# Kernel tuning notes

Hardware: AMD Instinct MI355X
Metric: run time of the kernel (lower is better)

## Reference

```python
import jax, jax.numpy as jnp
import numpy as np

N, E, F, D, EH, G, L, NG = 50000, 800000, 32, 32, 96, 128, 3, 500


def setup_inputs() -> dict:
    key = jax.random.key(0)
    ks = iter(jax.random.split(key, 32))
    w = lambda shape: jax.random.normal(next(ks), shape, dtype=jnp.float32) * 0.05
    inp = {
        "node_features": jax.random.normal(next(ks), (N, F), dtype=jnp.float32),
        "enc_W": w((F, D)), "enc_b": w((D,)),
        "msg_W1": w((L, 2 * D, EH)), "msg_b1": w((L, EH)),
        "msg_W2": w((L, EH, EH)), "msg_b2": w((L, EH)),
        "rmsg_W1": w((L, 2 * D, EH)), "rmsg_b1": w((L, EH)),
        "rmsg_W2": w((L, EH, EH)), "rmsg_b2": w((L, EH)),
        "gru_Wih": w((L, 3 * D, EH)), "gru_Whh": w((L, 3 * D, D)),
        "gru_bih": w((L, 3 * D)), "gru_bhh": w((L, 3 * D)),
        "agg_W1": w((D, 2 * G)), "agg_b1": w((2 * G,)),
        "agg_W2": w((G, G)), "agg_b2": w((G,)),
        "from_idx": jax.random.randint(next(ks), (E,), 0, N),
        "to_idx": jax.random.randint(next(ks), (E,), 0, N),
        "graph_idx": jnp.sort(jax.random.randint(next(ks), (N,), 0, NG)),
        "n_graphs": NG,
    }
    return inp


def _mlp(x, W1, b1, W2, b2):
    # Linear -> ReLU -> Linear (message net)
    return jax.nn.relu(x @ W1 + b1) @ W2 + b2


def _gru_step(x, h, Wih, Whh, bih, bhh):
    # torch nn.GRU single-step, gate order r, z, n
    gi = x @ Wih.T + bih  # [n, 3D]
    gh = h @ Whh.T + bhh  # [n, 3D]
    ir, iz, inn = jnp.split(gi, 3, axis=-1)
    hr, hz, hn = jnp.split(gh, 3, axis=-1)
    r = jax.nn.sigmoid(ir + hr)
    z = jax.nn.sigmoid(iz + hz)
    n = jnp.tanh(inn + r * hn)
    return (1.0 - z) * n + z * h


def _forward(node_features, enc_W, enc_b, msg_W1, msg_b1, msg_W2, msg_b2,
             rmsg_W1, rmsg_b1, rmsg_W2, rmsg_b2, gru_Wih, gru_Whh, gru_bih, gru_bhh,
             agg_W1, agg_b1, agg_W2, agg_b2, from_idx, to_idx, graph_idx, n_graphs):
    # GraphEncoder: single Linear
    h = node_features @ enc_W + enc_b  # [N, D]
    n_nodes = h.shape[0]
    n_layers = msg_W1.shape[0]
    for l in range(n_layers):  # small fixed layer count
        fs = h[from_idx]  # [E, D] gather
        ts = h[to_idx]    # [E, D] gather
        # forward-direction messages: gather -> concat -> MLP -> scatter_add to to_idx
        m = _mlp(jnp.concatenate([fs, ts], axis=-1), msg_W1[l], msg_b1[l], msg_W2[l], msg_b2[l])
        agg = jax.ops.segment_sum(m, to_idx, num_segments=n_nodes)
        # reverse direction: roles of from/to swapped, scatter to from_idx
        mr = _mlp(jnp.concatenate([ts, fs], axis=-1), rmsg_W1[l], rmsg_b1[l], rmsg_W2[l], rmsg_b2[l])
        agg = agg + jax.ops.segment_sum(mr, from_idx, num_segments=n_nodes)
        # node update via GRU (aggregated messages as input, node states as hidden)
        h = _gru_step(agg, h, gru_Wih[l], gru_Whh[l], gru_bih[l], gru_bhh[l])
    # GraphAggregator: gated node transform + scatter_add by graph, then Linear
    g = h @ agg_W1 + agg_b1  # [N, 2G]
    gdim = agg_W2.shape[0]
    gated = jax.nn.sigmoid(g[:, :gdim]) * g[:, gdim:]
    graph_states = jax.ops.segment_sum(gated, graph_idx, num_segments=n_graphs)  # [n_graphs, G]
    return graph_states @ agg_W2 + agg_b2


def reference(node_features, enc_W, enc_b, msg_W1, msg_b1, msg_W2, msg_b2,
              rmsg_W1, rmsg_b1, rmsg_W2, rmsg_b2, gru_Wih, gru_Whh, gru_bih, gru_bhh,
              agg_W1, agg_b1, agg_W2, agg_b2, from_idx, to_idx, graph_idx, n_graphs):
    return _forward(node_features, enc_W, enc_b, msg_W1, msg_b1, msg_W2, msg_b2,
                    rmsg_W1, rmsg_b1, rmsg_W2, rmsg_b2, gru_Wih, gru_Whh, gru_bih, gru_bhh,
                    agg_W1, agg_b1, agg_W2, agg_b2, from_idx, to_idx, graph_idx, n_graphs)
```

## Files before the change

### kernel.cpp

```cpp
#include <hip/hip_runtime.h>

#define SB 512

typedef __attribute__((ext_vector_type(8))) short short8;
typedef __attribute__((ext_vector_type(4))) float f32x4;

__device__ inline unsigned short f2bf(float f) {
    unsigned u = __float_as_uint(f);
    unsigned r = (u + 0x7fffu + ((u >> 16) & 1u)) >> 16;
    return (unsigned short)r;
}
__device__ inline unsigned pack2bf(float x, float y) {
    return (unsigned)f2bf(x) | ((unsigned)f2bf(y) << 16);
}

__global__ void count_rank_kernel(const int* __restrict__ from_idx, const int* __restrict__ to_idx,
                                  int* __restrict__ cnt_to, int* __restrict__ cnt_from,
                                  int* __restrict__ rank_to, int* __restrict__ rank_from, int E) {
    int e = blockIdx.x * blockDim.x + threadIdx.x;
    if (e >= E) return;
    int f = from_idx[e], t = to_idx[e];
    rank_to[e] = atomicAdd(&cnt_to[t], 1);
    rank_from[e] = atomicAdd(&cnt_from[f], 1);
}

__global__ void __launch_bounds__(SB) scanA_kernel(const int* __restrict__ cnt_to,
                                                   const int* __restrict__ cnt_from,
                                                   int* __restrict__ bsum, int nblk, int N) {
    const int* cnt = blockIdx.y ? cnt_from : cnt_to;
    __shared__ int s[SB];
    int tid = threadIdx.x;
    int i = blockIdx.x * SB + tid;
    s[tid] = (i < N) ? cnt[i] : 0;
    __syncthreads();
    for (int d = SB / 2; d > 0; d >>= 1) {
        if (tid < d) s[tid] += s[tid + d];
        __syncthreads();
    }
    if (tid == 0) bsum[blockIdx.y * nblk + blockIdx.x] = s[0];
}

__global__ void scanB_kernel(int* __restrict__ bsum, int* __restrict__ bbase,
                             int* __restrict__ off_to, int* __restrict__ off_from,
                             int nblk, int N) {
    int tid = threadIdx.x;
    if (tid < 2) {
        const int* bs = bsum + tid * nblk;
        int* bb = bbase + tid * nblk;
        int run = 0;
        for (int i = 0; i < nblk; ++i) { bb[i] = run; run += bs[i]; }
        if (tid == 0) off_to[N] = run; else off_from[N] = run;
    }
}

__global__ void __launch_bounds__(SB) scanC_kernel(const int* __restrict__ cnt_to,
                                                   const int* __restrict__ cnt_from,
                                                   const int* __restrict__ bbase,
                                                   int* __restrict__ off_to, int* __restrict__ off_from,
                                                   int nblk, int N) {
    const int* cnt = blockIdx.y ? cnt_from : cnt_to;
    int* off = blockIdx.y ? off_from : off_to;
    __shared__ int s[SB];
    int tid = threadIdx.x;
    int i = blockIdx.x * SB + tid;
    int v = (i < N) ? cnt[i] : 0;
    s[tid] = v;
    __syncthreads();
    for (int d = 1; d < SB; d <<= 1) {
        int t = s[tid];
        int add = (tid >= d) ? s[tid - d] : 0;
        __syncthreads();
        s[tid] = t + add;
        __syncthreads();
    }
    if (i < N) off[i] = s[tid] - v + bbase[blockIdx.y * nblk + blockIdx.x];
}

__global__ void fill_kernel(const int* __restrict__ from_idx, const int* __restrict__ to_idx,
                            const int* __restrict__ off_to, const int* __restrict__ off_from,
                            const int* __restrict__ rank_to, const int* __restrict__ rank_from,
                            int* __restrict__ list_to, int* __restrict__ list_from, int E) {
    int e = blockIdx.x * blockDim.x + threadIdx.x;
    if (e >= E) return;
    int f = from_idx[e], t = to_idx[e];
    list_to[off_to[t] + rank_to[e]] = f;
    list_from[off_from[f] + rank_from[e]] = t;
}

__global__ void transpose_whh(const float* __restrict__ Whh, float* __restrict__ WhhT) {
    int idx = blockIdx.x * 256 + threadIdx.x;
    if (idx >= 3 * 32 * 96) return;
    int l = idx / 3072, r = idx % 3072;
    int j = r / 96, k = r % 96;
    WhhT[idx] = Whh[l * 3072 + k * 32 + j];
}

__global__ void compose_kernel(const float* __restrict__ W2, const float* __restrict__ rW2,
                               const float* __restrict__ Wih,
                               const float* __restrict__ b2, const float* __restrict__ rb2,
                               float* __restrict__ M1, float* __restrict__ M2,
                               float* __restrict__ v12) {
    int l = blockIdx.x / 97, j = blockIdx.x % 97;
    int k = threadIdx.x;
    const float* wih = Wih + l * 9216 + k * 96;
    if (j < 96) {
        const float* w2  = W2 + l * 9216 + j * 96;
        const float* rw2 = rW2 + l * 9216 + j * 96;
        float a1 = 0.f, a2 = 0.f;
        for (int m = 0; m < 96; ++m) {
            float wv = wih[m];
            a1 = fmaf(w2[m], wv, a1);
            a2 = fmaf(rw2[m], wv, a2);
        }
        M1[l * 9216 + j * 96 + k] = a1;
        M2[l * 9216 + j * 96 + k] = a2;
    } else {
        const float* bb = b2 + l * 96;
        const float* rbb = rb2 + l * 96;
        float a1 = 0.f, a2 = 0.f;
        for (int m = 0; m < 96; ++m) {
            float wv = wih[m];
            a1 = fmaf(bb[m], wv, a1);
            a2 = fmaf(rbb[m], wv, a2);
        }
        v12[l * 192 + k] = a1;
        v12[l * 192 + 96 + k] = a2;
    }
}

__global__ void repack_kernel(const float* __restrict__ M1, const float* __restrict__ M2,
                              const float* __restrict__ WhhT,
                              const float* __restrict__ W1f, const float* __restrict__ W1r,
                              unsigned* __restrict__ M1bc, unsigned* __restrict__ M2bc,
                              unsigned* __restrict__ Whhbc, unsigned* __restrict__ W1bc) {
    int idx = blockIdx.x * 256 + threadIdx.x;
    if (idx < 13824) {
        int l = idx / 4608, r = idx % 4608, c = r / 48, wd = r % 48;
        const float* src = M1 + l * 9216;
        M1bc[idx] = pack2bf(src[(2 * wd) * 96 + c], src[(2 * wd + 1) * 96 + c]);
    } else if (idx < 27648) {
        int j = idx - 13824;
        int l = j / 4608, r = j % 4608, c = r / 48, wd = r % 48;
        const float* src = M2 + l * 9216;
        M2bc[j] = pack2bf(src[(2 * wd) * 96 + c], src[(2 * wd + 1) * 96 + c]);
    } else if (idx < 32256) {
        int j = idx - 27648;
        int l = j / 1536, r = j % 1536, c = r / 16, wd = r % 16;
        const float* src = WhhT + l * 3072;
        Whhbc[j] = pack2bf(src[(2 * wd) * 96 + c], src[(2 * wd + 1) * 96 + c]);
    } else if (idx < 32256 + 18432) {
        int j = idx - 32256;
        int l = j / 6144, r = j % 6144, C = r / 16, wd = r % 16;
        const float* src; int col, rb;
        if (C < 96)       { src = W1f + l * 6144; col = C;       rb = 0;  }
        else if (C < 192) { src = W1f + l * 6144; col = C - 96;  rb = 32; }
        else if (C < 288) { src = W1r + l * 6144; col = C - 192; rb = 0;  }
        else              { src = W1r + l * 6144; col = C - 288; rb = 32; }
        W1bc[j] = pack2bf(src[(rb + 2 * wd) * 96 + col], src[(rb + 2 * wd + 1) * 96 + col]);
    }
}

__global__ void __launch_bounds__(256) enc_gemm(const float* __restrict__ IN,
                                                const float* __restrict__ W, const float* __restrict__ bias,
                                                float* __restrict__ OUT, unsigned short* __restrict__ hb16, int N) {
    __shared__ float tile[64][33];
    int n0 = blockIdx.x * 64, tid = threadIdx.x;
    for (int idx = tid; idx < 64 * 32; idx += 256) {
        int r = idx >> 5, c = idx & 31;
        int n = n0 + r;
        tile[r][c] = (n < N) ? IN[(long)n * 32 + c] : 0.f;
    }
    __syncthreads();
    int lane = tid & 63;
    int w = __builtin_amdgcn_readfirstlane(tid >> 6);
    float acc[8] = {0};
    const float* Wp = W + w * 8;
#pragma unroll 4
    for (int j = 0; j < 32; ++j) {
        float a = tile[lane][j];
#pragma unroll
        for (int c = 0; c < 8; ++c) acc[c] = fmaf(a, Wp[j * 32 + c], acc[c]);
    }
    int n = n0 + lane;
    if (n >= N) return;
    float* outp = OUT + (long)n * 32 + w * 8;
    unsigned short* bp = hb16 + (long)n * 32 + w * 8;
#pragma unroll
    for (int c = 0; c < 8; ++c) {
        float v = acc[c] + bias[w * 8 + c];
        outp[c] = v;
        bp[c] = f2bf(v);
    }
}

__global__ void __launch_bounds__(512) proj_mfma(
    const unsigned* __restrict__ hb, const unsigned* __restrict__ W1bc,
    const float* __restrict__ b1f, const float* __restrict__ b1r,
    unsigned short* __restrict__ PaF16, float* __restrict__ PbF,
    unsigned short* __restrict__ PaR16, float* __restrict__ PbR, int N)
{
    int tid = threadIdx.x;
    int lane = tid & 63;
    int w = __builtin_amdgcn_readfirstlane(tid >> 6);
    int nt = w >> 1, cg = w & 1;
    int kgrp = lane >> 4, l15 = lane & 15;
    int ntile = blockIdx.x * 64 + nt * 16;
    int arow = ntile + l15;
    long arc = (arow < N) ? arow : (N - 1);
    short8 a = *(const short8*)(hb + arc * 16 + kgrp * 4);

    unsigned short* Pa16 = cg ? PaR16 : PaF16;
    float* Pb = cg ? PbR : PbF;
    const float* b1 = cg ? b1r : b1f;

    f32x4 acc[12];
#pragma unroll
    for (int ct = 0; ct < 12; ++ct) {
        int col = cg * 192 + ct * 16 + l15;
        short8 b = *(const short8*)(W1bc + (long)col * 16 + kgrp * 4);
        acc[ct] = __builtin_amdgcn_mfma_f32_16x16x32_bf16(a, b, (f32x4){0.f,0.f,0.f,0.f}, 0, 0, 0);
    }
    int nbase = ntile + kgrp * 4;
#pragma unroll
    for (int ct = 0; ct < 6; ++ct) {
        int col = ct * 16 + l15;
#pragma unroll
        for (int i = 0; i < 4; ++i) {
            int n = nbase + i;
            if (n < N) Pa16[(long)n * 96 + col] = f2bf(acc[ct][i]);
        }
    }
#pragma unroll
    for (int ct = 6; ct < 12; ++ct) {
        int col = (ct - 6) * 16 + l15;
        float bv = b1[col];
#pragma unroll
        for (int i = 0; i < 4; ++i) {
            int n = nbase + i;
            if (n < N) Pb[(long)n * 96 + col] = acc[ct][i] + bv;
        }
    }
}

__global__ void __launch_bounds__(256) agg_bf16(
    const int* __restrict__ offF, const int* __restrict__ listF,
    const int* __restrict__ offR, const int* __restrict__ listR,
    const unsigned* __restrict__ PaF, const unsigned* __restrict__ PaR,
    const float* __restrict__ PbF, const float* __restrict__ PbR,
    unsigned* __restrict__ AFb, unsigned* __restrict__ ARb, int N)
{
    const int* off; const int* list; const unsigned* Pa; const float* Pb; unsigned* AB;
    if (blockIdx.y == 0) { off = offF; list = listF; Pa = PaF; Pb = PbF; AB = AFb; }
    else                 { off = offR; list = listR; Pa = PaR; Pb = PbR; AB = ARb; }
    int n = __builtin_amdgcn_readfirstlane((blockIdx.x * 256 + threadIdx.x) >> 6);
    int lane = threadIdx.x & 63;
    if (n >= N) return;
    int li = (lane < 48) ? lane : 47;
    bool act = lane < 48;
    float sx = 0.f, sy = 0.f;
    if (act) { float2 s = *(const float2*)(Pb + (long)n * 96 + 2 * li); sx = s.x; sy = s.y; }
    float a0 = 0.f, a1 = 0.f;
    int beg = off[n], end = off[n + 1];
    int i = beg;
    for (; i + 8 <= end; i += 8) {
        unsigned u[8];
#pragma unroll
        for (int q = 0; q < 8; ++q) u[q] = Pa[(long)list[i + q] * 48 + li];
#pragma unroll
        for (int q = 0; q < 8; ++q) {
            a0 += fmaxf(__uint_as_float(u[q] << 16) + sx, 0.f);
            a1 += fmaxf(__uint_as_float(u[q] & 0xffff0000u) + sy, 0.f);
        }
    }
    for (; i < end; ++i) {
        unsigned u = Pa[(long)list[i] * 48 + li];
        a0 += fmaxf(__uint_as_float(u << 16) + sx, 0.f);
        a1 += fmaxf(__uint_as_float(u & 0xffff0000u) + sy, 0.f);
    }
    if (act) AB[(long)n * 48 + li] = pack2bf(a0, a1);
}

__global__ void __launch_bounds__(512) gru3_kernel(
    const unsigned* __restrict__ AFb, const unsigned* __restrict__ ARb,
    const unsigned* __restrict__ M1bc, const unsigned* __restrict__ M2bc,
    const unsigned* __restrict__ Whhbc,
    const float* __restrict__ v12,
    const int* __restrict__ offF, const int* __restrict__ offR,
    const float* __restrict__ h, const unsigned* __restrict__ hb,
    const float* __restrict__ bih, const float* __restrict__ bhh,
    float* __restrict__ hout, unsigned short* __restrict__ hbout, int N)
{
    int tid = threadIdx.x;
    int lane = tid & 63;
    int w = __builtin_amdgcn_readfirstlane(tid >> 6);
    int nt = w >> 1, cg = w & 1;
    int kgrp = lane >> 4;
    int c = cg * 16 + (lane & 15);
    int ntile = blockIdx.x * 64 + nt * 16;
    int arow = ntile + (lane & 15);
    long arc = (arow < N) ? arow : (N - 1);

    f32x4 acc[3]; f32x4 gh[3];
#pragma unroll
    for (int g = 0; g < 3; ++g) { acc[g] = (f32x4){0.f,0.f,0.f,0.f}; gh[g] = (f32x4){0.f,0.f,0.f,0.f}; }

    const unsigned* afp = AFb + arc * 48 + kgrp * 4;
    const unsigned* arp = ARb + arc * 48 + kgrp * 4;
#pragma unroll
    for (int k0 = 0; k0 < 3; ++k0) {
        short8 a = *(const short8*)(afp + k0 * 16);
#pragma unroll
        for (int g = 0; g < 3; ++g) {
            int col = g * 32 + c;
            short8 b = *(const short8*)(M1bc + (long)col * 48 + k0 * 16 + kgrp * 4);
            acc[g] = __builtin_amdgcn_mfma_f32_16x16x32_bf16(a, b, acc[g], 0, 0, 0);
        }
    }
#pragma unroll
    for (int k0 = 0; k0 < 3; ++k0) {
        short8 a = *(const short8*)(arp + k0 * 16);
#pragma unroll
        for (int g = 0; g < 3; ++g) {
            int col = g * 32 + c;
            short8 b = *(const short8*)(M2bc + (long)col * 48 + k0 * 16 + kgrp * 4);
            acc[g] = __builtin_amdgcn_mfma_f32_16x16x32_bf16(a, b, acc[g], 0, 0, 0);
        }
    }
    {
        short8 ha = *(const short8*)(hb + arc * 16 + kgrp * 4);
#pragma unroll
        for (int g = 0; g < 3; ++g) {
            int col = g * 32 + c;
            short8 b = *(const short8*)(Whhbc + (long)col * 16 + kgrp * 4);
            gh[g] = __builtin_amdgcn_mfma_f32_16x16x32_bf16(ha, b, gh[g], 0, 0, 0);
        }
    }

    float v1r[3], v2r[3], bihv[3], bhhv[3];
#pragma unroll
    for (int g = 0; g < 3; ++g) {
        int col = g * 32 + c;
        v1r[g] = v12[col]; v2r[g] = v12[96 + col];
        bihv[g] = bih[col]; bhhv[g] = bhh[col];
    }
    int nbase = ntile + kgrp * 4;
#pragma unroll
    for (int i = 0; i < 4; ++i) {
        int n = nbase + i;
        if (n < N) {
            float dF = (float)(offF[n + 1] - offF[n]);
            float dR = (float)(offR[n + 1] - offR[n]);
            float gir = acc[0][i] + dF * v1r[0] + dR * v2r[0] + bihv[0];
            float giz = acc[1][i] + dF * v1r[1] + dR * v2r[1] + bihv[1];
            float gin = acc[2][i] + dF * v1r[2] + dR * v2r[2] + bihv[2];
            float r = 1.f / (1.f + __expf(-(gir + gh[0][i] + bhhv[0])));
            float z = 1.f / (1.f + __expf(-(giz + gh[1][i] + bhhv[1])));
            float nn = tanhf(gin + r * (gh[2][i] + bhhv[2]));
            float hv = h[(long)n * 32 + c];
            float vout = (1.f - z) * nn + z * hv;
            hout[(long)n * 32 + c] = vout;
            hbout[(long)n * 32 + c] = f2bf(vout);
        }
    }
}

__global__ void __launch_bounds__(128) graph_agg(const float* __restrict__ h, const float* __restrict__ W1,
                          const float* __restrict__ b1, const int* __restrict__ gidx,
                          float* __restrict__ gs, int N, int chunk) {
    int k = threadIdx.x;
    int n_start = blockIdx.x * chunk;
    if (n_start >= N) return;
    int n_end = min(n_start + chunk, N);
    float w1[32], w2[32];
#pragma unroll
    for (int j = 0; j < 32; ++j) {
        w1[j] = W1[j * 256 + k];
        w2[j] = W1[j * 256 + 128 + k];
    }
    float bb1 = b1[k], bb2 = b1[128 + k];
    float acc = 0.f;
    int cur = gidx[n_start];
    for (int n = n_start; n < n_end; ++n) {
        int g = gidx[n];
        if (g != cur) { atomicAdd(&gs[cur * 128 + k], acc); acc = 0.f; cur = g; }
        float g1 = bb1, g2 = bb2;
#pragma unroll
        for (int j = 0; j < 32; ++j) {
            float hv = h[(long)n * 32 + j];
            g1 = fmaf(hv, w1[j], g1);
            g2 = fmaf(hv, w2[j], g2);
        }
        acc += (1.f / (1.f + __expf(-g1))) * g2;
    }
    atomicAdd(&gs[cur * 128 + k], acc);
}

__global__ void final_gemm(const float* __restrict__ gs, const float* __restrict__ W,
                           const float* __restrict__ b, float* __restrict__ out) {
    int g = blockIdx.x, k = threadIdx.x;
    float a = b[k];
#pragma unroll 8
    for (int j = 0; j < 128; ++j) a = fmaf(gs[g * 128 + j], W[j * 128 + k], a);
    out[g * 128 + k] = a;
}

extern "C" void kernel_launch(void* const* d_in, const int* in_sizes, int n_in,
                              void* d_out, int out_size, void* d_ws, size_t ws_size,
                              hipStream_t stream) {
    const float* node_features = (const float*)d_in[0];
    const float* enc_W  = (const float*)d_in[1];
    const float* enc_b  = (const float*)d_in[2];
    const float* msg_W1 = (const float*)d_in[3];
    const float* msg_b1 = (const float*)d_in[4];
    const float* msg_W2 = (const float*)d_in[5];
    const float* msg_b2 = (const float*)d_in[6];
    const float* rmsg_W1 = (const float*)d_in[7];
    const float* rmsg_b1 = (const float*)d_in[8];
    const float* rmsg_W2 = (const float*)d_in[9];
    const float* rmsg_b2 = (const float*)d_in[10];
    const float* gru_Wih = (const float*)d_in[11];
    const float* gru_Whh = (const float*)d_in[12];
    const float* gru_bih = (const float*)d_in[13];
    const float* gru_bhh = (const float*)d_in[14];
    const float* agg_W1 = (const float*)d_in[15];
    const float* agg_b1 = (const float*)d_in[16];
    const float* agg_W2 = (const float*)d_in[17];
    const float* agg_b2 = (const float*)d_in[18];
    const int* from_idx = (const int*)d_in[19];
    const int* to_idx   = (const int*)d_in[20];
    const int* graph_idx = (const int*)d_in[21];

    const int N = in_sizes[0] / 32;
    const int E = in_sizes[19];
    const int NG = out_size / 128;
    float* out = (float*)d_out;

    char* ws = (char*)d_ws;
    auto alloc = [&](size_t b) { void* p = (void*)ws; ws += (b + 255) & ~(size_t)255; return p; };
    int* cnt_to   = (int*)alloc((size_t)N * 4);
    int* cnt_from = (int*)alloc((size_t)N * 4);
    int* off_to   = (int*)alloc((size_t)(N + 1) * 4);
    int* off_from = (int*)alloc((size_t)(N + 1) * 4);
    int* list_to  = (int*)alloc((size_t)E * 4);
    int* list_from= (int*)alloc((size_t)E * 4);
    float* h0  = (float*)alloc((size_t)N * 32 * 4);
    float* h1  = (float*)alloc((size_t)N * 32 * 4);
    unsigned* PaF = (unsigned*)alloc((size_t)N * 48 * 4);
    unsigned* PaR = (unsigned*)alloc((size_t)N * 48 * 4);
    float* PbF = (float*)alloc((size_t)N * 96 * 4);
    float* PbR = (float*)alloc((size_t)N * 96 * 4);
    unsigned* AFb = (unsigned*)alloc((size_t)N * 48 * 4);
    unsigned* ARb = (unsigned*)alloc((size_t)N * 48 * 4);
    unsigned* hb0 = (unsigned*)alloc((size_t)N * 16 * 4);
    unsigned* hb1 = (unsigned*)alloc((size_t)N * 16 * 4);
    float* WhhT = (float*)alloc((size_t)3 * 32 * 96 * 4);
    float* M1   = (float*)alloc((size_t)3 * 96 * 96 * 4);
    float* M2   = (float*)alloc((size_t)3 * 96 * 96 * 4);
    float* v12  = (float*)alloc((size_t)3 * 192 * 4);
    unsigned* M1bc = (unsigned*)alloc((size_t)13824 * 4);
    unsigned* M2bc = (unsigned*)alloc((size_t)13824 * 4);
    unsigned* Whhbc = (unsigned*)alloc((size_t)4608 * 4);
    unsigned* W1bc  = (unsigned*)alloc((size_t)18432 * 4);
    float* gs   = (float*)alloc((size_t)NG * 128 * 4);
    const int nblk = (N + SB - 1) / SB;
    int* bsum  = (int*)alloc((size_t)2 * nblk * 4);
    int* bbase = (int*)alloc((size_t)2 * nblk * 4);
    int* rank_to   = (int*)PbF;
    int* rank_from = (int*)PbR;

    hipMemsetAsync(cnt_to, 0, (size_t)N * 4, stream);
    hipMemsetAsync(cnt_from, 0, (size_t)N * 4, stream);
    hipMemsetAsync(gs, 0, (size_t)NG * 128 * 4, stream);

    int gE = (E + 255) / 256;
    count_rank_kernel<<<gE, 256, 0, stream>>>(from_idx, to_idx, cnt_to, cnt_from, rank_to, rank_from, E);
    dim3 gScan(nblk, 2);
    scanA_kernel<<<gScan, SB, 0, stream>>>(cnt_to, cnt_from, bsum, nblk, N);
    scanB_kernel<<<1, 64, 0, stream>>>(bsum, bbase, off_to, off_from, nblk, N);
    scanC_kernel<<<gScan, SB, 0, stream>>>(cnt_to, cnt_from, bbase, off_to, off_from, nblk, N);
    fill_kernel<<<gE, 256, 0, stream>>>(from_idx, to_idx, off_to, off_from, rank_to, rank_from,
                                        list_to, list_from, E);

    transpose_whh<<<(3 * 32 * 96 + 255) / 256, 256, 0, stream>>>(gru_Whh, WhhT);
    compose_kernel<<<3 * 97, 96, 0, stream>>>(msg_W2, rmsg_W2, gru_Wih, msg_b2, rmsg_b2, M1, M2, v12);
    repack_kernel<<<(32256 + 18432 + 255) / 256, 256, 0, stream>>>(M1, M2, WhhT, msg_W1, rmsg_W1,
                                                                   M1bc, M2bc, Whhbc, W1bc);

    int gN64 = (N + 63) / 64;
    enc_gemm<<<gN64, 256, 0, stream>>>(node_features, enc_W, enc_b, h0, (unsigned short*)hb0, N);

    float* hcur = h0; float* hnext = h1;
    unsigned* hbcur = hb0; unsigned* hbnext = hb1;
    dim3 gAgg((N + 3) / 4, 2);
    for (int l = 0; l < 3; ++l) {
        proj_mfma<<<gN64, 512, 0, stream>>>(hbcur, W1bc + l * 6144,
                                            msg_b1 + l * 96, rmsg_b1 + l * 96,
                                            (unsigned short*)PaF, PbF, (unsigned short*)PaR, PbR, N);
        agg_bf16<<<gAgg, 256, 0, stream>>>(off_to, list_to, off_from, list_from,
                                           PaF, PaR, PbF, PbR, AFb, ARb, N);
        gru3_kernel<<<gN64, 512, 0, stream>>>(AFb, ARb, M1bc + l * 4608, M2bc + l * 4608,
                                              Whhbc + l * 1536, v12 + l * 192,
                                              off_to, off_from, hcur, hbcur,
                                              gru_bih + l * 96, gru_bhh + l * 96, hnext,
                                              (unsigned short*)hbnext, N);
        float* t = hcur; hcur = hnext; hnext = t;
        unsigned* tb = hbcur; hbcur = hbnext; hbnext = tb;
    }

    const int chunk = 32;
    graph_agg<<<(N + chunk - 1) / chunk, 128, 0, stream>>>(hcur, agg_W1, agg_b1, graph_idx, gs, N, chunk);
    final_gemm<<<NG, 128, 0, stream>>>(gs, agg_W2, agg_b2, out);
}
```

Measured before the change: 436.4 us.

## Fuse forward/reverse edge aggregation into one pass and store Pb in bf16

```diff
diff --git a/kernel.cpp b/kernel.cpp
--- a/kernel.cpp
+++ b/kernel.cpp
@@ -87,14 +87,6 @@
     list_from[off_from[f] + rank_from[e]] = t;
 }
 
-__global__ void transpose_whh(const float* __restrict__ Whh, float* __restrict__ WhhT) {
-    int idx = blockIdx.x * 256 + threadIdx.x;
-    if (idx >= 3 * 32 * 96) return;
-    int l = idx / 3072, r = idx % 3072;
-    int j = r / 96, k = r % 96;
-    WhhT[idx] = Whh[l * 3072 + k * 32 + j];
-}
-
 __global__ void compose_kernel(const float* __restrict__ W2, const float* __restrict__ rW2,
                                const float* __restrict__ Wih,
                                const float* __restrict__ b2, const float* __restrict__ rb2,
@@ -129,7 +121,7 @@
 }
 
 __global__ void repack_kernel(const float* __restrict__ M1, const float* __restrict__ M2,
-                              const float* __restrict__ WhhT,
+                              const float* __restrict__ Whh,
                               const float* __restrict__ W1f, const float* __restrict__ W1r,
                               unsigned* __restrict__ M1bc, unsigned* __restrict__ M2bc,
                               unsigned* __restrict__ Whhbc, unsigned* __restrict__ W1bc) {
@@ -146,8 +138,8 @@
     } else if (idx < 32256) {
         int j = idx - 27648;
         int l = j / 1536, r = j % 1536, c = r / 16, wd = r % 16;
-        const float* src = WhhT + l * 3072;
-        Whhbc[j] = pack2bf(src[(2 * wd) * 96 + c], src[(2 * wd + 1) * 96 + c]);
+        const float* src = Whh + l * 3072 + c * 32;
+        Whhbc[j] = pack2bf(src[2 * wd], src[2 * wd + 1]);
     } else if (idx < 32256 + 18432) {
         int j = idx - 32256;
         int l = j / 6144, r = j % 6144, C = r / 16, wd = r % 16;
@@ -196,8 +188,8 @@
 __global__ void __launch_bounds__(512) proj_mfma(
     const unsigned* __restrict__ hb, const unsigned* __restrict__ W1bc,
     const float* __restrict__ b1f, const float* __restrict__ b1r,
-    unsigned short* __restrict__ PaF16, float* __restrict__ PbF,
-    unsigned short* __restrict__ PaR16, float* __restrict__ PbR, int N)
+    unsigned short* __restrict__ PaF16, unsigned short* __restrict__ PbF16,
+    unsigned short* __restrict__ PaR16, unsigned short* __restrict__ PbR16, int N)
 {
     int tid = threadIdx.x;
     int lane = tid & 63;
@@ -210,7 +202,7 @@
     short8 a = *(const short8*)(hb + arc * 16 + kgrp * 4);
 
     unsigned short* Pa16 = cg ? PaR16 : PaF16;
-    float* Pb = cg ? PbR : PbF;
+    unsigned short* Pb16 = cg ? PbR16 : PbF16;
     const float* b1 = cg ? b1r : b1f;
 
     f32x4 acc[12];
@@ -237,47 +229,83 @@
 #pragma unroll
         for (int i = 0; i < 4; ++i) {
             int n = nbase + i;
-            if (n < N) Pb[(long)n * 96 + col] = acc[ct][i] + bv;
-        }
-    }
-}
-
-__global__ void __launch_bounds__(256) agg_bf16(
+            if (n < N) Pb16[(long)n * 96 + col] = f2bf(acc[ct][i] + bv);
+        }
+    }
+}
+
+__global__ void __launch_bounds__(256) agg_dual(
     const int* __restrict__ offF, const int* __restrict__ listF,
     const int* __restrict__ offR, const int* __restrict__ listR,
     const unsigned* __restrict__ PaF, const unsigned* __restrict__ PaR,
-    const float* __restrict__ PbF, const float* __restrict__ PbR,
+    const unsigned short* __restrict__ PbF16, const unsigned short* __restrict__ PbR16,
     unsigned* __restrict__ AFb, unsigned* __restrict__ ARb, int N)
 {
-    const int* off; const int* list; const unsigned* Pa; const float* Pb; unsigned* AB;
-    if (blockIdx.y == 0) { off = offF; list = listF; Pa = PaF; Pb = PbF; AB = AFb; }
-    else                 { off = offR; list = listR; Pa = PaR; Pb = PbR; AB = ARb; }
     int n = __builtin_amdgcn_readfirstlane((blockIdx.x * 256 + threadIdx.x) >> 6);
     int lane = threadIdx.x & 63;
     if (n >= N) return;
     int li = (lane < 48) ? lane : 47;
     bool act = lane < 48;
-    float sx = 0.f, sy = 0.f;
-    if (act) { float2 s = *(const float2*)(Pb + (long)n * 96 + 2 * li); sx = s.x; sy = s.y; }
-    float a0 = 0.f, a1 = 0.f;
-    int beg = off[n], end = off[n + 1];
-    int i = beg;
-    for (; i + 8 <= end; i += 8) {
+    float sxF = 0.f, syF = 0.f, sxR = 0.f, syR = 0.f;
+    if (act) {
+        unsigned sF = *(const unsigned*)(PbF16 + (long)n * 96 + 2 * li);
+        unsigned sR = *(const unsigned*)(PbR16 + (long)n * 96 + 2 * li);
+        sxF = __uint_as_float(sF << 16); syF = __uint_as_float(sF & 0xffff0000u);
+        sxR = __uint_as_float(sR << 16); syR = __uint_as_float(sR & 0xffff0000u);
+    }
+    float f0 = 0.f, f1 = 0.f, r0 = 0.f, r1 = 0.f;
+    int begF = offF[n], endF = offF[n + 1];
+    int begR = offR[n], endR = offR[n + 1];
+    int iF = begF, iR = begR;
+    while (iF + 8 <= endF && iR + 8 <= endR) {
+        unsigned uF[8], uR[8];
+#pragma unroll
+        for (int q = 0; q < 8; ++q) uF[q] = PaF[(long)listF[iF + q] * 48 + li];
+#pragma unroll
+        for (int q = 0; q < 8; ++q) uR[q] = PaR[(long)listR[iR + q] * 48 + li];
+#pragma unroll
+        for (int q = 0; q < 8; ++q) {
+            f0 += fmaxf(__uint_as_float(uF[q] << 16) + sxF, 0.f);
+            f1 += fmaxf(__uint_as_float(uF[q] & 0xffff0000u) + syF, 0.f);
+            r0 += fmaxf(__uint_as_float(uR[q] << 16) + sxR, 0.f);
+            r1 += fmaxf(__uint_as_float(uR[q] & 0xffff0000u) + syR, 0.f);
+        }
+        iF += 8; iR += 8;
+    }
+    for (; iF + 8 <= endF; iF += 8) {
         unsigned u[8];
 #pragma unroll
-        for (int q = 0; q < 8; ++q) u[q] = Pa[(long)list[i + q] * 48 + li];
+        for (int q = 0; q < 8; ++q) u[q] = PaF[(long)listF[iF + q] * 48 + li];
 #pragma unroll
         for (int q = 0; q < 8; ++q) {
-            a0 += fmaxf(__uint_as_float(u[q] << 16) + sx, 0.f);
-            a1 += fmaxf(__uint_as_float(u[q] & 0xffff0000u) + sy, 0.f);
-        }
-    }
-    for (; i < end; ++i) {
-        unsigned u = Pa[(long)list[i] * 48 + li];
-        a0 += fmaxf(__uint_as_float(u << 16) + sx, 0.f);
-        a1 += fmaxf(__uint_as_float(u & 0xffff0000u) + sy, 0.f);
-    }
-    if (act) AB[(long)n * 48 + li] = pack2bf(a0, a1);
+            f0 += fmaxf(__uint_as_float(u[q] << 16) + sxF, 0.f);
+            f1 += fmaxf(__uint_as_float(u[q] & 0xffff0000u) + syF, 0.f);
+        }
+    }
+    for (; iR + 8 <= endR; iR += 8) {
+        unsigned u[8];
+#pragma unroll
+        for (int q = 0; q < 8; ++q) u[q] = PaR[(long)listR[iR + q] * 48 + li];
+#pragma unroll
+        for (int q = 0; q < 8; ++q) {
+            r0 += fmaxf(__uint_as_float(u[q] << 16) + sxR, 0.f);
+            r1 += fmaxf(__uint_as_float(u[q] & 0xffff0000u) + syR, 0.f);
+        }
+    }
+    for (; iF < endF; ++iF) {
+        unsigned u = PaF[(long)listF[iF] * 48 + li];
+        f0 += fmaxf(__uint_as_float(u << 16) + sxF, 0.f);
+        f1 += fmaxf(__uint_as_float(u & 0xffff0000u) + syF, 0.f);
+    }
+    for (; iR < endR; ++iR) {
+        unsigned u = PaR[(long)listR[iR] * 48 + li];
+        r0 += fmaxf(__uint_as_float(u << 16) + sxR, 0.f);
+        r1 += fmaxf(__uint_as_float(u & 0xffff0000u) + syR, 0.f);
+    }
+    if (act) {
+        AFb[(long)n * 48 + li] = pack2bf(f0, f1);
+        ARb[(long)n * 48 + li] = pack2bf(r0, r1);
+    }
 }
 
 __global__ void __launch_bounds__(512) gru3_kernel(
@@ -447,13 +475,12 @@
     float* h1  = (float*)alloc((size_t)N * 32 * 4);
     unsigned* PaF = (unsigned*)alloc((size_t)N * 48 * 4);
     unsigned* PaR = (unsigned*)alloc((size_t)N * 48 * 4);
-    float* PbF = (float*)alloc((size_t)N * 96 * 4);
-    float* PbR = (float*)alloc((size_t)N * 96 * 4);
+    unsigned short* PbF16 = (unsigned short*)alloc((size_t)N * 96 * 2);
+    unsigned short* PbR16 = (unsigned short*)alloc((size_t)N * 96 * 2);
     unsigned* AFb = (unsigned*)alloc((size_t)N * 48 * 4);
     unsigned* ARb = (unsigned*)alloc((size_t)N * 48 * 4);
     unsigned* hb0 = (unsigned*)alloc((size_t)N * 16 * 4);
     unsigned* hb1 = (unsigned*)alloc((size_t)N * 16 * 4);
-    float* WhhT = (float*)alloc((size_t)3 * 32 * 96 * 4);
     float* M1   = (float*)alloc((size_t)3 * 96 * 96 * 4);
     float* M2   = (float*)alloc((size_t)3 * 96 * 96 * 4);
     float* v12  = (float*)alloc((size_t)3 * 192 * 4);
@@ -465,8 +492,8 @@
     const int nblk = (N + SB - 1) / SB;
     int* bsum  = (int*)alloc((size_t)2 * nblk * 4);
     int* bbase = (int*)alloc((size_t)2 * nblk * 4);
-    int* rank_to   = (int*)PbF;
-    int* rank_from = (int*)PbR;
+    int* rank_to   = (int*)PaF;
+    int* rank_from = (int*)PaR;
 
     hipMemsetAsync(cnt_to, 0, (size_t)N * 4, stream);
     hipMemsetAsync(cnt_from, 0, (size_t)N * 4, stream);
@@ -481,9 +508,8 @@
     fill_kernel<<<gE, 256, 0, stream>>>(from_idx, to_idx, off_to, off_from, rank_to, rank_from,
                                         list_to, list_from, E);
 
-    transpose_whh<<<(3 * 32 * 96 + 255) / 256, 256, 0, stream>>>(gru_Whh, WhhT);
     compose_kernel<<<3 * 97, 96, 0, stream>>>(msg_W2, rmsg_W2, gru_Wih, msg_b2, rmsg_b2, M1, M2, v12);
-    repack_kernel<<<(32256 + 18432 + 255) / 256, 256, 0, stream>>>(M1, M2, WhhT, msg_W1, rmsg_W1,
+    repack_kernel<<<(32256 + 18432 + 255) / 256, 256, 0, stream>>>(M1, M2, gru_Whh, msg_W1, rmsg_W1,
                                                                    M1bc, M2bc, Whhbc, W1bc);
 
     int gN64 = (N + 63) / 64;
@@ -491,13 +517,13 @@
 
     float* hcur = h0; float* hnext = h1;
     unsigned* hbcur = hb0; unsigned* hbnext = hb1;
-    dim3 gAgg((N + 3) / 4, 2);
+    int gAgg = (N + 3) / 4;
     for (int l = 0; l < 3; ++l) {
         proj_mfma<<<gN64, 512, 0, stream>>>(hbcur, W1bc + l * 6144,
                                             msg_b1 + l * 96, rmsg_b1 + l * 96,
-                                            (unsigned short*)PaF, PbF, (unsigned short*)PaR, PbR, N);
-        agg_bf16<<<gAgg, 256, 0, stream>>>(off_to, list_to, off_from, list_from,
-                                           PaF, PaR, PbF, PbR, AFb, ARb, N);
+                                            (unsigned short*)PaF, PbF16, (unsigned short*)PaR, PbR16, N);
+        agg_dual<<<gAgg, 256, 0, stream>>>(off_to, list_to, off_from, list_from,
+                                           PaF, PaR, PbF16, PbR16, AFb, ARb, N);
         gru3_kernel<<<gN64, 512, 0, stream>>>(AFb, ARb, M1bc + l * 4608, M2bc + l * 4608,
                                               Whhbc + l * 1536, v12 + l * 192,
                                               off_to, off_from, hcur, hbcur,
```

Result: no change. 443.5 us (+1.6%).

## Store Pb projection in bf16, drop Whh transpose kernel, mask agg tail loop

Applied to the files above, without the earlier changes.

```diff
diff --git a/kernel.cpp b/kernel.cpp
--- a/kernel.cpp
+++ b/kernel.cpp
@@ -87,14 +87,6 @@
     list_from[off_from[f] + rank_from[e]] = t;
 }
 
-__global__ void transpose_whh(const float* __restrict__ Whh, float* __restrict__ WhhT) {
-    int idx = blockIdx.x * 256 + threadIdx.x;
-    if (idx >= 3 * 32 * 96) return;
-    int l = idx / 3072, r = idx % 3072;
-    int j = r / 96, k = r % 96;
-    WhhT[idx] = Whh[l * 3072 + k * 32 + j];
-}
-
 __global__ void compose_kernel(const float* __restrict__ W2, const float* __restrict__ rW2,
                                const float* __restrict__ Wih,
                                const float* __restrict__ b2, const float* __restrict__ rb2,
@@ -129,7 +121,7 @@
 }
 
 __global__ void repack_kernel(const float* __restrict__ M1, const float* __restrict__ M2,
-                              const float* __restrict__ WhhT,
+                              const float* __restrict__ Whh,
                               const float* __restrict__ W1f, const float* __restrict__ W1r,
                               unsigned* __restrict__ M1bc, unsigned* __restrict__ M2bc,
                               unsigned* __restrict__ Whhbc, unsigned* __restrict__ W1bc) {
@@ -146,8 +138,8 @@
     } else if (idx < 32256) {
         int j = idx - 27648;
         int l = j / 1536, r = j % 1536, c = r / 16, wd = r % 16;
-        const float* src = WhhT + l * 3072;
-        Whhbc[j] = pack2bf(src[(2 * wd) * 96 + c], src[(2 * wd + 1) * 96 + c]);
+        const float* src = Whh + l * 3072 + c * 32;
+        Whhbc[j] = pack2bf(src[2 * wd], src[2 * wd + 1]);
     } else if (idx < 32256 + 18432) {
         int j = idx - 32256;
         int l = j / 6144, r = j % 6144, C = r / 16, wd = r % 16;
@@ -196,8 +188,8 @@
 __global__ void __launch_bounds__(512) proj_mfma(
     const unsigned* __restrict__ hb, const unsigned* __restrict__ W1bc,
     const float* __restrict__ b1f, const float* __restrict__ b1r,
-    unsigned short* __restrict__ PaF16, float* __restrict__ PbF,
-    unsigned short* __restrict__ PaR16, float* __restrict__ PbR, int N)
+    unsigned short* __restrict__ PaF16, unsigned short* __restrict__ PbF16,
+    unsigned short* __restrict__ PaR16, unsigned short* __restrict__ PbR16, int N)
 {
     int tid = threadIdx.x;
     int lane = tid & 63;
@@ -210,7 +202,7 @@
     short8 a = *(const short8*)(hb + arc * 16 + kgrp * 4);
 
     unsigned short* Pa16 = cg ? PaR16 : PaF16;
-    float* Pb = cg ? PbR : PbF;
+    unsigned short* Pb16 = cg ? PbR16 : PbF16;
     const float* b1 = cg ? b1r : b1f;
 
     f32x4 acc[12];
@@ -237,7 +229,7 @@
 #pragma unroll
         for (int i = 0; i < 4; ++i) {
             int n = nbase + i;
-            if (n < N) Pb[(long)n * 96 + col] = acc[ct][i] + bv;
+            if (n < N) Pb16[(long)n * 96 + col] = f2bf(acc[ct][i] + bv);
         }
     }
 }
@@ -246,36 +238,44 @@
     const int* __restrict__ offF, const int* __restrict__ listF,
     const int* __restrict__ offR, const int* __restrict__ listR,
     const unsigned* __restrict__ PaF, const unsigned* __restrict__ PaR,
-    const float* __restrict__ PbF, const float* __restrict__ PbR,
+    const unsigned short* __restrict__ PbF16, const unsigned short* __restrict__ PbR16,
     unsigned* __restrict__ AFb, unsigned* __restrict__ ARb, int N)
 {
-    const int* off; const int* list; const unsigned* Pa; const float* Pb; unsigned* AB;
-    if (blockIdx.y == 0) { off = offF; list = listF; Pa = PaF; Pb = PbF; AB = AFb; }
-    else                 { off = offR; list = listR; Pa = PaR; Pb = PbR; AB = ARb; }
+    const int* off; const int* list; const unsigned* Pa; const unsigned short* Pb16; unsigned* AB;
+    if (blockIdx.y == 0) { off = offF; list = listF; Pa = PaF; Pb16 = PbF16; AB = AFb; }
+    else                 { off = offR; list = listR; Pa = PaR; Pb16 = PbR16; AB = ARb; }
     int n = __builtin_amdgcn_readfirstlane((blockIdx.x * 256 + threadIdx.x) >> 6);
     int lane = threadIdx.x & 63;
     if (n >= N) return;
     int li = (lane < 48) ? lane : 47;
     bool act = lane < 48;
     float sx = 0.f, sy = 0.f;
-    if (act) { float2 s = *(const float2*)(Pb + (long)n * 96 + 2 * li); sx = s.x; sy = s.y; }
+    if (act) {
+        unsigned s = *(const unsigned*)(Pb16 + (long)n * 96 + 2 * li);
+        sx = __uint_as_float(s << 16);
+        sy = __uint_as_float(s & 0xffff0000u);
+    }
     float a0 = 0.f, a1 = 0.f;
     int beg = off[n], end = off[n + 1];
-    int i = beg;
-    for (; i + 8 <= end; i += 8) {
-        unsigned u[8];
-#pragma unroll
-        for (int q = 0; q < 8; ++q) u[q] = Pa[(long)list[i + q] * 48 + li];
-#pragma unroll
-        for (int q = 0; q < 8; ++q) {
-            a0 += fmaxf(__uint_as_float(u[q] << 16) + sx, 0.f);
-            a1 += fmaxf(__uint_as_float(u[q] & 0xffff0000u) + sy, 0.f);
-        }
-    }
-    for (; i < end; ++i) {
-        unsigned u = Pa[(long)list[i] * 48 + li];
-        a0 += fmaxf(__uint_as_float(u << 16) + sx, 0.f);
-        a1 += fmaxf(__uint_as_float(u & 0xffff0000u) + sy, 0.f);
+    if (end > beg) {
+        int nb = (end - beg + 7) >> 3;
+        for (int b = 0; b < nb; ++b) {
+            int base = beg + b * 8;
+            unsigned u[8]; float m[8];
+#pragma unroll
+            for (int q = 0; q < 8; ++q) {
+                int idx = base + q;
+                bool v = idx < end;
+                int src = list[v ? idx : end - 1];
+                u[q] = Pa[(long)src * 48 + li];
+                m[q] = v ? 1.f : 0.f;
+            }
+#pragma unroll
+            for (int q = 0; q < 8; ++q) {
+                a0 += m[q] * fmaxf(__uint_as_float(u[q] << 16) + sx, 0.f);
+                a1 += m[q] * fmaxf(__uint_as_float(u[q] & 0xffff0000u) + sy, 0.f);
+            }
+        }
     }
     if (act) AB[(long)n * 48 + li] = pack2bf(a0, a1);
 }
@@ -447,13 +447,12 @@
     float* h1  = (float*)alloc((size_t)N * 32 * 4);
     unsigned* PaF = (unsigned*)alloc((size_t)N * 48 * 4);
     unsigned* PaR = (unsigned*)alloc((size_t)N * 48 * 4);
-    float* PbF = (float*)alloc((size_t)N * 96 * 4);
-    float* PbR = (float*)alloc((size_t)N * 96 * 4);
+    unsigned short* PbF16 = (unsigned short*)alloc((size_t)N * 96 * 2);
+    unsigned short* PbR16 = (unsigned short*)alloc((size_t)N * 96 * 2);
     unsigned* AFb = (unsigned*)alloc((size_t)N * 48 * 4);
     unsigned* ARb = (unsigned*)alloc((size_t)N * 48 * 4);
     unsigned* hb0 = (unsigned*)alloc((size_t)N * 16 * 4);
     unsigned* hb1 = (unsigned*)alloc((size_t)N * 16 * 4);
-    float* WhhT = (float*)alloc((size_t)3 * 32 * 96 * 4);
     float* M1   = (float*)alloc((size_t)3 * 96 * 96 * 4);
     float* M2   = (float*)alloc((size_t)3 * 96 * 96 * 4);
     float* v12  = (float*)alloc((size_t)3 * 192 * 4);
@@ -465,8 +464,8 @@
     const int nblk = (N + SB - 1) / SB;
     int* bsum  = (int*)alloc((size_t)2 * nblk * 4);
     int* bbase = (int*)alloc((size_t)2 * nblk * 4);
-    int* rank_to   = (int*)PbF;
-    int* rank_from = (int*)PbR;
+    int* rank_to   = (int*)PaF;
+    int* rank_from = (int*)PaR;
 
     hipMemsetAsync(cnt_to, 0, (size_t)N * 4, stream);
     hipMemsetAsync(cnt_from, 0, (size_t)N * 4, stream);
@@ -481,9 +480,8 @@
     fill_kernel<<<gE, 256, 0, stream>>>(from_idx, to_idx, off_to, off_from, rank_to, rank_from,
                                         list_to, list_from, E);
 
-    transpose_whh<<<(3 * 32 * 96 + 255) / 256, 256, 0, stream>>>(gru_Whh, WhhT);
     compose_kernel<<<3 * 97, 96, 0, stream>>>(msg_W2, rmsg_W2, gru_Wih, msg_b2, rmsg_b2, M1, M2, v12);
-    repack_kernel<<<(32256 + 18432 + 255) / 256, 256, 0, stream>>>(M1, M2, WhhT, msg_W1, rmsg_W1,
+    repack_kernel<<<(32256 + 18432 + 255) / 256, 256, 0, stream>>>(M1, M2, gru_Whh, msg_W1, rmsg_W1,
                                                                    M1bc, M2bc, Whhbc, W1bc);
 
     int gN64 = (N + 63) / 64;
@@ -495,9 +493,9 @@
     for (int l = 0; l < 3; ++l) {
         proj_mfma<<<gN64, 512, 0, stream>>>(hbcur, W1bc + l * 6144,
                                             msg_b1 + l * 96, rmsg_b1 + l * 96,
-                                            (unsigned short*)PaF, PbF, (unsigned short*)PaR, PbR, N);
+                                            (unsigned short*)PaF, PbF16, (unsigned short*)PaR, PbR16, N);
         agg_bf16<<<gAgg, 256, 0, stream>>>(off_to, list_to, off_from, list_from,
-                                           PaF, PaR, PbF, PbR, AFb, ARb, N);
+                                           PaF, PaR, PbF16, PbR16, AFb, ARb, N);
         gru3_kernel<<<gN64, 512, 0, stream>>>(AFb, ARb, M1bc + l * 4608, M2bc + l * 4608,
                                               Whhbc + l * 1536, v12 + l * 192,
                                               off_to, off_from, hcur, hbcur,
```

Result: no change. 431.2 us (-1.2%).
